# Kernel optimization log

Measured on AMD Instinct MI355X. Metric: run time of the kernel, lower is better.

The kernel has to match this reference:

```python
import jax, jax.numpy as jnp
import numpy as np

EPS = 1e-12

def cont_6d_to_rmat(d6):
    # d6: (..., 6) -> (..., 3, 3); standard Zhou et al. continuous 6D representation
    a1, a2 = d6[..., :3], d6[..., 3:]
    b1 = a1 / jnp.clip(jnp.linalg.norm(a1, axis=-1, keepdims=True), EPS)
    a2p = a2 - jnp.sum(b1 * a2, axis=-1, keepdims=True) * b1
    b2 = a2p / jnp.clip(jnp.linalg.norm(a2p, axis=-1, keepdims=True), EPS)
    b3 = jnp.cross(b1, b2)
    return jnp.stack([b1, b2, b3], axis=-1)  # b1,b2,b3 are columns


def setup_inputs() -> dict:
    key = jax.random.key(0)
    k1, k2, k3, k4, k5 = jax.random.split(key, 5)
    G, K, F, B = 400000, 20, 300, 8
    return {
        "motion_rots": jax.random.normal(k1, (K, F, 6), dtype=jnp.float32),
        "motion_transls": jax.random.normal(k2, (K, F, 3), dtype=jnp.float32),
        "motion_coefs": jax.random.normal(k3, (G, K), dtype=jnp.float32),
        "means": jax.random.normal(k4, (G, 3), dtype=jnp.float32),
        "ts": jax.random.randint(k5, (B,), 0, F),
    }


def reference(motion_rots, motion_transls, motion_coefs, means, ts):
    # compute_transforms
    mt = jnp.swapaxes(motion_transls[:, ts], 0, 1)          # (B, K, 3)
    mr = motion_rots[:, ts]                                  # (K, B, 6)
    coefs = jax.nn.softmax(motion_coefs, axis=-1)            # (G, K)
    transls = jnp.einsum('pk,nki->pni', coefs, mt)           # (G, B, 3)
    rots = jnp.einsum('pk,kni->pni', coefs, mr)              # (G, B, 6)
    rotmats = cont_6d_to_rmat(rots)                          # (G, B, 3, 3)
    transfms = jnp.concatenate([rotmats, transls[..., None]], axis=-1)  # (G, B, 3, 4)
    # compute_means: apply homogeneous transform to padded means
    means_h = jnp.concatenate([means, jnp.ones_like(means[:, :1])], axis=-1)  # (G, 4)
    return jnp.einsum('pnij,pj->pni', transfms, means_h)     # (G, B, 3)
```

## Files before the change

### kernel.cpp

```cpp
#include <hip/hip_runtime.h>


constexpr int KK    = 20;
constexpr int BB    = 8;
constexpr int BLK   = 256;
constexpr int GPB   = 64;
constexpr int SLICE = 9 * KK;

typedef __attribute__((ext_vector_type(2))) float f32x2;

__global__ void gather_tab(const float* __restrict__ motion_rots,
                           const float* __restrict__ motion_transls,
                           const int*   __restrict__ ts,
                           float* __restrict__ tab,
                           int F)
{
    const int tid = threadIdx.x;
    if (tid < BB * KK) {
        const int n = tid / KK, k = tid % KK;
        const int t = ts[n];
        const float* rp = motion_rots    + ((size_t)k * F + t) * 6;
        const float* tp = motion_transls + ((size_t)k * F + t) * 3;
        float* base = tab + (size_t)n * SLICE;
        #pragma unroll
        for (int c = 0; c < 6; ++c) base[c * KK + k] = rp[c];
        #pragma unroll
        for (int c = 0; c < 3; ++c) base[(6 + c) * KK + k] = tp[c];
    }
}

__global__ __launch_bounds__(BLK) void motion_fwd(
    const float* __restrict__ motion_coefs,
    const float* __restrict__ means,
    const float* __restrict__ tab,
    float* __restrict__ out,
    int G)
{
    const int tid  = threadIdx.x;
    const int q    = __builtin_amdgcn_readfirstlane(tid >> 6);
    const int lane = tid & 63;
    const long long p  = (long long)blockIdx.x * GPB + lane;
    const long long pc = p < G ? p : (long long)G - 1;

    f32x2 w2[10];
    float invs;
    {
        const float4* crow = reinterpret_cast<const float4*>(motion_coefs + pc * KK);
        float s = 0.f;
        #pragma unroll
        for (int u = 0; u < 5; ++u) {
            const float4 v = crow[u];
            const float e0 = __expf(v.x), e1 = __expf(v.y);
            const float e2 = __expf(v.z), e3 = __expf(v.w);
            w2[2*u+0] = (f32x2){e0, e1};
            w2[2*u+1] = (f32x2){e2, e3};
            s += (e0 + e1) + (e2 + e3);
        }
        invs = __builtin_amdgcn_rcpf(s);
    }
    const float mx0 = means[pc*3+0], mx1 = means[pc*3+1], mx2 = means[pc*3+2];

    auto do_slice = [&](int sl) {
        const float* tb = tab + (size_t)sl * SLICE;

        f32x2 acc[9];
        #pragma unroll
        for (int c = 0; c < 9; ++c) acc[c] = (f32x2){0.f, 0.f};

        #pragma unroll
        for (int c = 0; c < 9; ++c) {
            #pragma unroll
            for (int kk = 0; kk < 10; ++kk) {
                const f32x2 t = *reinterpret_cast<const f32x2*>(tb + c * KK + 2 * kk);
                acc[c] += w2[kk] * t;
            }
        }

        float r[9];
        #pragma unroll
        for (int c = 0; c < 9; ++c) r[c] = acc[c].x + acc[c].y;

        const float n1 = __builtin_amdgcn_sqrtf(fmaf(r[0], r[0], fmaf(r[1], r[1], r[2]*r[2])));
        const float i1 = __builtin_amdgcn_rcpf(fmaxf(n1, 1e-12f));
        const float b10 = r[0]*i1, b11 = r[1]*i1, b12 = r[2]*i1;

        const float d  = fmaf(b10, r[3], fmaf(b11, r[4], b12*r[5]));
        const float q0 = fmaf(-d, b10, r[3]);
        const float q1 = fmaf(-d, b11, r[4]);
        const float q2 = fmaf(-d, b12, r[5]);
        const float n2 = __builtin_amdgcn_sqrtf(fmaf(q0, q0, fmaf(q1, q1, q2*q2)));
        const float i2 = __builtin_amdgcn_rcpf(fmaxf(n2, 1e-12f));
        const float b20 = q0*i2, b21 = q1*i2, b22 = q2*i2;

        const float b30 = fmaf(b11, b22, -(b12*b21));
        const float b31 = fmaf(b12, b20, -(b10*b22));
        const float b32 = fmaf(b10, b21, -(b11*b20));

        const float u0 = r[6] * invs;
        const float u1 = r[7] * invs;
        const float u2 = r[8] * invs;

        const float o0 = fmaf(b10, mx0, fmaf(b20, mx1, fmaf(b30, mx2, u0)));
        const float o1 = fmaf(b11, mx0, fmaf(b21, mx1, fmaf(b31, mx2, u1)));
        const float o2 = fmaf(b12, mx0, fmaf(b22, mx1, fmaf(b32, mx2, u2)));

        if (p < G) {
            float* op = out + (size_t)p * (BB*3) + (size_t)sl * 3;
            op[0] = o0; op[1] = o1; op[2] = o2;
        }
    };

    do_slice(q);
    do_slice(q + 4);
}

extern "C" void kernel_launch(void* const* d_in, const int* in_sizes, int n_in,
                              void* d_out, int out_size, void* d_ws, size_t ws_size,
                              hipStream_t stream) {
    const float* motion_rots    = (const float*)d_in[0];
    const float* motion_transls = (const float*)d_in[1];
    const float* motion_coefs   = (const float*)d_in[2];
    const float* means          = (const float*)d_in[3];
    const int*   ts             = (const int*)d_in[4];
    float* out = (float*)d_out;
    float* tab = (float*)d_ws;

    const int G = in_sizes[3] / 3;
    const int F = in_sizes[0] / (6 * KK);

    gather_tab<<<1, 192, 0, stream>>>(motion_rots, motion_transls, ts, tab, F);

    const int nblk = (G + GPB - 1) / GPB;
    motion_fwd<<<nblk, BLK, 0, stream>>>(motion_coefs, means, tab, out, G);
}
```

Measured before the change: 34.75 us.

## Use one wave per time slice and share softmax weights via LDS

New measurement: 35.22 us. Within noise of the previous version (+1.4%).

```diff
diff --git a/kernel.cpp b/kernel.cpp
--- a/kernel.cpp
+++ b/kernel.cpp
@@ -3,7 +3,7 @@
 
 constexpr int KK    = 20;
 constexpr int BB    = 8;
-constexpr int BLK   = 256;
+constexpr int BLK   = 64 * BB;
 constexpr int GPB   = 64;
 constexpr int SLICE = 9 * KK;
 
@@ -36,15 +36,16 @@
     float* __restrict__ out,
     int G)
 {
+    __shared__ f32x2 wp_lds[KK / 2][64];
+    __shared__ float winv_lds[64];
+
     const int tid  = threadIdx.x;
-    const int q    = __builtin_amdgcn_readfirstlane(tid >> 6);
+    const int wq   = __builtin_amdgcn_readfirstlane(tid >> 6);
     const int lane = tid & 63;
     const long long p  = (long long)blockIdx.x * GPB + lane;
     const long long pc = p < G ? p : (long long)G - 1;
 
-    f32x2 w2[10];
-    float invs;
-    {
+    if (wq == 0) {
         const float4* crow = reinterpret_cast<const float4*>(motion_coefs + pc * KK);
         float s = 0.f;
         #pragma unroll
@@ -52,66 +53,67 @@
             const float4 v = crow[u];
             const float e0 = __expf(v.x), e1 = __expf(v.y);
             const float e2 = __expf(v.z), e3 = __expf(v.w);
-            w2[2*u+0] = (f32x2){e0, e1};
-            w2[2*u+1] = (f32x2){e2, e3};
+            wp_lds[2*u+0][lane] = (f32x2){e0, e1};
+            wp_lds[2*u+1][lane] = (f32x2){e2, e3};
             s += (e0 + e1) + (e2 + e3);
         }
-        invs = __builtin_amdgcn_rcpf(s);
+        winv_lds[lane] = __builtin_amdgcn_rcpf(s);
     }
+    __syncthreads();
+
+    f32x2 w2[KK / 2];
+    #pragma unroll
+    for (int kk = 0; kk < KK / 2; ++kk) w2[kk] = wp_lds[kk][lane];
+    const float invs = winv_lds[lane];
     const float mx0 = means[pc*3+0], mx1 = means[pc*3+1], mx2 = means[pc*3+2];
 
-    auto do_slice = [&](int sl) {
-        const float* tb = tab + (size_t)sl * SLICE;
+    const float* tb = tab + (size_t)wq * SLICE;
 
-        f32x2 acc[9];
+    f32x2 acc[9];
+    #pragma unroll
+    for (int c = 0; c < 9; ++c) acc[c] = (f32x2){0.f, 0.f};
+
+    #pragma unroll
+    for (int c = 0; c < 9; ++c) {
         #pragma unroll
-        for (int c = 0; c < 9; ++c) acc[c] = (f32x2){0.f, 0.f};
+        for (int kk = 0; kk < KK / 2; ++kk) {
+            const f32x2 t = *reinterpret_cast<const f32x2*>(tb + c * KK + 2 * kk);
+            acc[c] += w2[kk] * t;
+        }
+    }
 
-        #pragma unroll
-        for (int c = 0; c < 9; ++c) {
-            #pragma unroll
-            for (int kk = 0; kk < 10; ++kk) {
-                const f32x2 t = *reinterpret_cast<const f32x2*>(tb + c * KK + 2 * kk);
-                acc[c] += w2[kk] * t;
-            }
-        }
+    float r[9];
+    #pragma unroll
+    for (int c = 0; c < 9; ++c) r[c] = acc[c].x + acc[c].y;
 
-        float r[9];
-        #pragma unroll
-        for (int c = 0; c < 9; ++c) r[c] = acc[c].x + acc[c].y;
+    const float n1 = __builtin_amdgcn_sqrtf(fmaf(r[0], r[0], fmaf(r[1], r[1], r[2]*r[2])));
+    const float i1 = __builtin_amdgcn_rcpf(fmaxf(n1, 1e-12f));
+    const float b10 = r[0]*i1, b11 = r[1]*i1, b12 = r[2]*i1;
 
-        const float n1 = __builtin_amdgcn_sqrtf(fmaf(r[0], r[0], fmaf(r[1], r[1], r[2]*r[2])));
-        const float i1 = __builtin_amdgcn_rcpf(fmaxf(n1, 1e-12f));
-        const float b10 = r[0]*i1, b11 = r[1]*i1, b12 = r[2]*i1;
+    const float d  = fmaf(b10, r[3], fmaf(b11, r[4], b12*r[5]));
+    const float q0 = fmaf(-d, b10, r[3]);
+    const float q1 = fmaf(-d, b11, r[4]);
+    const float q2 = fmaf(-d, b12, r[5]);
+    const float n2 = __builtin_amdgcn_sqrtf(fmaf(q0, q0, fmaf(q1, q1, q2*q2)));
+    const float i2 = __builtin_amdgcn_rcpf(fmaxf(n2, 1e-12f));
+    const float b20 = q0*i2, b21 = q1*i2, b22 = q2*i2;
 
-        const float d  = fmaf(b10, r[3], fmaf(b11, r[4], b12*r[5]));
-        const float q0 = fmaf(-d, b10, r[3]);
-        const float q1 = fmaf(-d, b11, r[4]);
-        const float q2 = fmaf(-d, b12, r[5]);
-        const float n2 = __builtin_amdgcn_sqrtf(fmaf(q0, q0, fmaf(q1, q1, q2*q2)));
-        const float i2 = __builtin_amdgcn_rcpf(fmaxf(n2, 1e-12f));
-        const float b20 = q0*i2, b21 = q1*i2, b22 = q2*i2;
+    const float b30 = fmaf(b11, b22, -(b12*b21));
+    const float b31 = fmaf(b12, b20, -(b10*b22));
+    const float b32 = fmaf(b10, b21, -(b11*b20));
 
-        const float b30 = fmaf(b11, b22, -(b12*b21));
-        const float b31 = fmaf(b12, b20, -(b10*b22));
-        const float b32 = fmaf(b10, b21, -(b11*b20));
+    const float u0 = r[6] * invs;
+    const float u1 = r[7] * invs;
+    const float u2 = r[8] * invs;
 
-        const float u0 = r[6] * invs;
-        const float u1 = r[7] * invs;
-        const float u2 = r[8] * invs;
+    const float o0 = fmaf(b10, mx0, fmaf(b20, mx1, fmaf(b30, mx2, u0)));
+    const float o1 = fmaf(b11, mx0, fmaf(b21, mx1, fmaf(b31, mx2, u1)));
+    const float o2 = fmaf(b12, mx0, fmaf(b22, mx1, fmaf(b32, mx2, u2)));
 
-        const float o0 = fmaf(b10, mx0, fmaf(b20, mx1, fmaf(b30, mx2, u0)));
-        const float o1 = fmaf(b11, mx0, fmaf(b21, mx1, fmaf(b31, mx2, u1)));
-        const float o2 = fmaf(b12, mx0, fmaf(b22, mx1, fmaf(b32, mx2, u2)));
-
-        if (p < G) {
-            float* op = out + (size_t)p * (BB*3) + (size_t)sl * 3;
-            op[0] = o0; op[1] = o1; op[2] = o2;
-        }
-    };
-
-    do_slice(q);
-    do_slice(q + 4);
+    if (p < G) {
+        float* op = out + (size_t)p * (BB*3) + (size_t)wq * 3;
+        op[0] = o0; op[1] = o1; op[2] = o2;
+    }
 }
 
 extern "C" void kernel_launch(void* const* d_in, const int* in_sizes, int n_in,
```
